# Optimization experiments

Hardware: AMD Instinct MI355X
Metric: run time of the kernel (lower is better)

The kernel has to match this reference:

```python
import jax, jax.numpy as jnp
import numpy as np

B, S, D = 2, 2048, 2048
NH, NKV, HD = 16, 4, 128
REP = NH // NKV
EPS = 1e-6
ROPE_THETA = 1e6


def setup_inputs() -> dict:
    key = jax.random.key(0)
    ks = jax.random.split(key, 6)
    x = jax.random.normal(ks[0], (B, S, D), jnp.float32)
    # real rotary embeddings: [S, HD]
    inv_freq = 1.0 / (ROPE_THETA ** (np.arange(0, HD, 2, dtype=np.float64) / HD))
    freqs = np.outer(np.arange(S, dtype=np.float64), inv_freq)
    emb = np.concatenate([freqs, freqs], axis=-1)
    cos = jnp.asarray(np.cos(emb), jnp.float32)
    sin = jnp.asarray(np.sin(emb), jnp.float32)
    scale = 1.0 / np.sqrt(D)
    Wq = jax.random.normal(ks[1], (D, NH * HD), jnp.float32) * scale   # [in, out]
    Wk = jax.random.normal(ks[2], (D, NKV * HD), jnp.float32) * scale
    Wv = jax.random.normal(ks[3], (D, NKV * HD), jnp.float32) * scale
    Wo = jax.random.normal(ks[4], (NH * HD, D), jnp.float32) * (1.0 / np.sqrt(NH * HD))
    q_norm_w = jnp.ones((HD,), jnp.float32)
    k_norm_w = jnp.ones((HD,), jnp.float32)
    return dict(x=x, cos=cos, sin=sin, Wq=Wq, Wk=Wk, Wv=Wv, Wo=Wo,
                q_norm_w=q_norm_w, k_norm_w=k_norm_w)


def _rms_norm(h, w):
    var = jnp.mean(h * h, axis=-1, keepdims=True)
    return w * (h * jax.lax.rsqrt(var + EPS))


def _rotate_half(h):
    h1, h2 = jnp.split(h, 2, axis=-1)
    return jnp.concatenate([-h2, h1], axis=-1)


def reference(x, cos, sin, Wq, Wk, Wv, Wo, q_norm_w, k_norm_w):
    b, s, _ = x.shape
    q = (x @ Wq).reshape(b, s, NH, HD)
    k = (x @ Wk).reshape(b, s, NKV, HD)
    v = (x @ Wv).reshape(b, s, NKV, HD)
    # per-head QK RMSNorm
    q = _rms_norm(q, q_norm_w)
    k = _rms_norm(k, k_norm_w)
    # RoPE: cos/sin [S,HD] -> broadcast over batch and heads
    c = cos[None, :, None, :]
    s_ = sin[None, :, None, :]
    q = q * c + _rotate_half(q) * s_
    k = k * c + _rotate_half(k) * s_
    # GQA: group q heads per kv head instead of materializing repeat_kv
    qg = q.reshape(b, s, NKV, REP, HD)
    scores = jnp.einsum('bqgrd,bkgd->bgrqk', qg, k) / np.sqrt(HD)
    causal = jnp.tril(jnp.ones((s, s), bool))  # [q,k]
    scores = jnp.where(causal, scores, -jnp.inf)
    probs = jax.nn.softmax(scores.astype(jnp.float32), axis=-1).astype(q.dtype)
    out = jnp.einsum('bgrqk,bkgd->bqgrd', probs, v).reshape(b, s, NH * HD)
    return out @ Wo
```

## Files before the change

kernel.cpp:

```cpp
#include <hip/hip_runtime.h>
#include <hip/hip_bf16.h>
#include <math.h>

#define B_ 2
#define S_ 2048
#define D_ 2048
#define NH_ 16
#define NKV_ 4
#define HD_ 128
#define EPS_ 1e-6f
#define SCALE_ 0.08838834764831845f
#define LOG2E_ 1.4426950408889634f
#define KOFF_ 2048
#define VOFF_ 2560
#define MINIT_ -1e30f

typedef float f32x4 __attribute__((ext_vector_type(4)));
typedef short bf16x8 __attribute__((ext_vector_type(8)));
typedef short short4v __attribute__((ext_vector_type(4)));
typedef float float4v __attribute__((ext_vector_type(4)));
typedef unsigned uint2v __attribute__((ext_vector_type(2)));
typedef unsigned uint4v __attribute__((ext_vector_type(4)));

static __device__ __forceinline__ short f2bf(float f) {
    union { float f; unsigned u; } x{f};
    unsigned r = (x.u + 0x7fff + ((x.u >> 16) & 1)) >> 16;
    return (short)r;
}
static __device__ __forceinline__ float bf2f(short s) {
    union { unsigned u; float f; } x; x.u = ((unsigned)(unsigned short)s) << 16; return x.f;
}
static __device__ __forceinline__ unsigned pack_bf2(float a, float b) {
    return __builtin_amdgcn_perm(__builtin_bit_cast(unsigned, b),
                                 __builtin_bit_cast(unsigned, a), 0x07060302u);
}

#define AS1(p) ((const __attribute__((address_space(1))) void*)(p))
#define AS3(p) ((__attribute__((address_space(3))) void*)(p))
static __device__ __forceinline__ void async16(const void* g, void* l) {
    __builtin_amdgcn_global_load_lds(AS1(g), AS3(l), 16, 0, 0);
}
#define SB_() __builtin_amdgcn_sched_barrier(0)

__global__ __launch_bounds__(256) void cast_kernel(const float* __restrict__ in,
                                                   short* __restrict__ out) {
    size_t i = ((size_t)blockIdx.x * 256 + threadIdx.x) * 4;
    float4v v = *(const float4v*)(in + i);
    short4v o; o.x = f2bf(v.x); o.y = f2bf(v.y); o.z = f2bf(v.z); o.w = f2bf(v.w);
    *(short4v*)(out + i) = o;
}

__global__ __launch_bounds__(256) void transpose_all_kernel(const float* __restrict__ Wq,
                                                            const float* __restrict__ Wk,
                                                            const float* __restrict__ Wv,
                                                            const float* __restrict__ Wo,
                                                            short* __restrict__ Wt,
                                                            short* __restrict__ Wot) {
    __shared__ float tile[64][65];
    const int bx = blockIdx.x, by = blockIdx.y;
    const float* src; short* dst; int N, nb;
    if (bx < 32)      { src = Wq; dst = Wt;                         N = 2048; nb = bx; }
    else if (bx < 40) { src = Wk; dst = Wt + (size_t)KOFF_ * 2048;  N = 512;  nb = bx - 32; }
    else if (bx < 48) { src = Wv; dst = Wt + (size_t)VOFF_ * 2048;  N = 512;  nb = bx - 40; }
    else              { src = Wo; dst = Wot;                        N = 2048; nb = bx - 48; }
    const int n0 = nb * 64, k0 = by * 64;
    const int tid = threadIdx.x;
    for (int r = 0; r < 16; ++r) {
        int k = r * 4 + (tid >> 6);
        int n = tid & 63;
        tile[k][n] = src[(size_t)(k0 + k) * N + n0 + n];
    }
    __syncthreads();
    for (int r = 0; r < 4; ++r) {
        int n  = r * 16 + (tid >> 4);
        int kk = (tid & 15) * 4;
        short4v o4;
        o4.x = f2bf(tile[kk + 0][n]); o4.y = f2bf(tile[kk + 1][n]);
        o4.z = f2bf(tile[kk + 2][n]); o4.w = f2bf(tile[kk + 3][n]);
        *(short4v*)&dst[(size_t)(n0 + n) * 2048 + k0 + kk] = o4;
    }
}

__global__ __launch_bounds__(512, 2) void gemm_oproj_kernel(const short* __restrict__ A,
                                                            const short* __restrict__ Bt,
                                                            float* __restrict__ C) {
    __shared__ __align__(16) short smem[49152];
    short* A0 = smem;
    short* A1 = smem + 8192;
    short* B0 = smem + 16384;
    short* B1 = smem + 32768;

    const int tid  = threadIdx.x;
    const int orig = blockIdx.y * 8 + blockIdx.x;
    const int swz  = (orig & 7) * 32 + (orig >> 3);
    const int bn = swz & 7, bm = swz >> 3;
    const int wave = tid >> 6, lane = tid & 63;
    const int quad = lane >> 4, l16 = lane & 15;
    const int wr = wave >> 2, wc = wave & 3;

    const short* Ag = A  + (size_t)(bm * 128) * 2048;
    const short* Bg = Bt + (size_t)(bn * 256) * 2048;

    f32x4 acc[4][4];
#pragma unroll
    for (int i = 0; i < 4; ++i)
#pragma unroll
        for (int j = 0; j < 4; ++j) acc[i][j] = (f32x4){0.f, 0.f, 0.f, 0.f};

    bf16x8 a[4][2], b0[2][2], b1[2][2];

    auto stage_half = [&](const short* gpanel, int t, int h, short* lslot) {
#pragma unroll
        for (int u = 0; u < 2; ++u) {
            int ci = u * 512 + tid;
            int r  = ci >> 3;
            int cb = ((ci & 7) * 16) ^ ((r & 7) << 4);
            async16(gpanel + (size_t)(h * 128 + r) * 2048 + t * 64 + (cb >> 1),
                    lslot + h * 8192 + ci * 8);
        }
    };

#define OLDA_(lbuf) \
    _Pragma("unroll") for (int mt = 0; mt < 4; ++mt) \
    _Pragma("unroll") for (int ks = 0; ks < 2; ++ks) { \
        int row_ = wr * 64 + mt * 16 + l16; \
        int cb_  = (ks * 64 + quad * 16) ^ ((row_ & 7) << 4); \
        a[mt][ks] = *(const bf16x8*)&(lbuf)[row_ * 64 + (cb_ >> 1)]; \
    }
#define OLDB_(lbuf, qn, breg) \
    _Pragma("unroll") for (int ntl = 0; ntl < 2; ++ntl) \
    _Pragma("unroll") for (int ks = 0; ks < 2; ++ks) { \
        int row_ = wc * 64 + (qn) * 32 + ntl * 16 + l16; \
        int cb_  = (ks * 64 + quad * 16) ^ ((row_ & 7) << 4); \
        breg[ntl][ks] = *(const bf16x8*)&(lbuf)[row_ * 64 + (cb_ >> 1)]; \
    }
#define OBAR_() __builtin_amdgcn_s_barrier()
#define OMFMA_(qn, breg) do { \
    __builtin_amdgcn_s_setprio(1); \
    _Pragma("unroll") for (int mt = 0; mt < 4; ++mt) \
    _Pragma("unroll") for (int ntl = 0; ntl < 2; ++ntl) \
    _Pragma("unroll") for (int ks = 0; ks < 2; ++ks) \
        acc[mt][(qn) * 2 + ntl] = __builtin_amdgcn_mfma_f32_16x16x32_bf16( \
            a[mt][ks], breg[ntl][ks], acc[mt][(qn) * 2 + ntl], 0, 0, 0); \
    __builtin_amdgcn_s_setprio(0); __builtin_amdgcn_s_barrier(); } while (0)

    stage_half(Bg, 0, 0, B0); stage_half(Bg, 0, 1, B0);
    stage_half(Ag, 0, 0, A0);
    asm volatile("s_waitcnt vmcnt(0)" ::: "memory");
    __builtin_amdgcn_s_barrier();

#pragma unroll 1
    for (int i = 0; i < 16; ++i) {
        const int tE = 2 * i, tO = 2 * i + 1;
        const bool more = (i < 15);

        stage_half(Ag, tO, 0, A1);
        stage_half(Bg, tO, 0, B1); stage_half(Bg, tO, 1, B1);
        OLDA_(A0); OLDB_(B0, 0, b0);
        OBAR_();
        OMFMA_(0, b0);

        if (more) {
            stage_half(Ag, tE + 2, 0, A0);
            asm volatile("s_waitcnt vmcnt(2)" ::: "memory");
        } else {
            asm volatile("s_waitcnt vmcnt(0)" ::: "memory");
        }
        OLDB_(B0, 1, b1);
        OBAR_();
        OMFMA_(1, b1);

        if (more) { stage_half(Bg, tE + 2, 0, B0); stage_half(Bg, tE + 2, 1, B0); }
        OLDA_(A1); OLDB_(B1, 0, b0);
        OBAR_();
        OMFMA_(0, b0);

        if (more) { asm volatile("s_waitcnt vmcnt(0)" ::: "memory"); }
        OLDB_(B1, 1, b1);
        OBAR_();
        OMFMA_(1, b1);
    }

#pragma unroll
    for (int mt = 0; mt < 4; ++mt)
#pragma unroll
        for (int nt = 0; nt < 4; ++nt)
#pragma unroll
            for (int j = 0; j < 4; ++j) {
                int row = bm * 128 + wr * 64 + mt * 16 + quad * 4 + j;
                int col = bn * 256 + wc * 64 + nt * 16 + l16;
                C[(size_t)row * 2048 + col] = acc[mt][nt][j];
            }
#undef OLDA_
#undef OLDB_
#undef OBAR_
#undef OMFMA_
}

#define QKV_ITERS 16

__global__ __launch_bounds__(512, 2) void qkv_fused_kernel(const short* __restrict__ xb,
                                                           const short* __restrict__ Wt,
                                                           const float* __restrict__ cosb,
                                                           const float* __restrict__ sinb,
                                                           const float* __restrict__ qw,
                                                           const float* __restrict__ kw,
                                                           short* __restrict__ q_rope,
                                                           short* __restrict__ k_rope,
                                                           short* __restrict__ vtr) {
    __shared__ __align__(16) short smem[65536];

    short* A0 = smem;
    short* A1 = smem + 8192;
    short* B0 = smem + 16384;
    short* B1 = smem + 40960;

    const int tid  = threadIdx.x;
    const int orig = blockIdx.y * 8 + blockIdx.x;
    const int swz  = (orig & 7) * 32 + (orig >> 3);
    const int bn = swz >> 5, bm = swz & 31;
    const int wave = tid >> 6, lane = tid & 63;
    const int quad = lane >> 4, l16 = lane & 15;
    const int wr = wave >> 2, wc = wave & 3;

    const short* Ag = xb + (size_t)(bm * 128) * 2048;
    const short* Bg = Wt + (size_t)(bn * 384) * 2048;

    f32x4 acc[4][6];
#pragma unroll
    for (int i = 0; i < 4; ++i)
#pragma unroll
        for (int j = 0; j < 6; ++j) acc[i][j] = (f32x4){0.f, 0.f, 0.f, 0.f};

    bf16x8 a[4][2], b0[3][2], b1[3][2];

    auto stage_half = [&](const short* gpanel, int t, int h, short* lslot) {
#pragma unroll
        for (int u = 0; u < 2; ++u) {
            int ci = u * 512 + tid;
            int r  = ci >> 3;
            int cb = ((ci & 7) * 16) ^ ((r & 7) << 4);
            async16(gpanel + (size_t)(h * 128 + r) * 2048 + t * 64 + (cb >> 1),
                    lslot + h * 8192 + ci * 8);
        }
    };

#define LDA_(lbuf) \
    _Pragma("unroll") for (int mt = 0; mt < 4; ++mt) \
    _Pragma("unroll") for (int ks = 0; ks < 2; ++ks) { \
        int row_ = wr * 64 + mt * 16 + l16; \
        int cb_  = (ks * 64 + quad * 16) ^ ((row_ & 7) << 4); \
        a[mt][ks] = *(const bf16x8*)&(lbuf)[row_ * 64 + (cb_ >> 1)]; \
    }
#define LDB_(lbuf, qn, breg) \
    _Pragma("unroll") for (int ntl = 0; ntl < 3; ++ntl) \
    _Pragma("unroll") for (int ks = 0; ks < 2; ++ks) { \
        int row_ = wc * 96 + (qn) * 48 + ntl * 16 + l16; \
        int cb_  = (ks * 64 + quad * 16) ^ ((row_ & 7) << 4); \
        breg[ntl][ks] = *(const bf16x8*)&(lbuf)[row_ * 64 + (cb_ >> 1)]; \
    }
#define PH_BAR() do { __builtin_amdgcn_sched_barrier(0); __builtin_amdgcn_s_barrier(); } while (0)
#define PH_MFMA24(qn, breg) do { \
        __builtin_amdgcn_s_setprio(1); \
        _Pragma("unroll") for (int mt = 0; mt < 4; ++mt) \
        _Pragma("unroll") for (int ntl = 0; ntl < 3; ++ntl) \
        _Pragma("unroll") for (int ks = 0; ks < 2; ++ks) \
            acc[mt][(qn) * 3 + ntl] = __builtin_amdgcn_mfma_f32_16x16x32_bf16( \
                a[mt][ks], breg[ntl][ks], acc[mt][(qn) * 3 + ntl], 0, 0, 0); \
        __builtin_amdgcn_s_setprio(0); \
        __builtin_amdgcn_sched_barrier(0); __builtin_amdgcn_s_barrier(); } while (0)

    stage_half(Bg, 0, 0, B0); stage_half(Bg, 0, 1, B0); stage_half(Bg, 0, 2, B0);
    stage_half(Ag, 0, 0, A0);
    stage_half(Ag, 1, 0, A1);
    asm volatile("s_waitcnt vmcnt(2)" ::: "memory");
    __builtin_amdgcn_s_barrier();

#pragma unroll 1
    for (int i = 0; i < QKV_ITERS; ++i) {
        const int tE = 2 * i, tO = 2 * i + 1;
        const bool more = (i < QKV_ITERS - 1);

        LDA_(A0); LDB_(B0, 0, b0);
        stage_half(Bg, tO, 0, B1); stage_half(Bg, tO, 1, B1); stage_half(Bg, tO, 2, B1);
        PH_BAR();
        PH_MFMA24(0, b0);

        LDB_(B0, 1, b1);
        if (more) {
            stage_half(Ag, tE + 2, 0, A0);
            asm volatile("s_waitcnt vmcnt(2)" ::: "memory");
        } else {
            asm volatile("s_waitcnt vmcnt(0)" ::: "memory");
        }
        PH_BAR();
        PH_MFMA24(1, b1);

        LDA_(A1); LDB_(B1, 0, b0);
        if (more) { stage_half(Bg, tE + 2, 0, B0); stage_half(Bg, tE + 2, 1, B0); stage_half(Bg, tE + 2, 2, B0); }
        PH_BAR();
        PH_MFMA24(0, b0);

        LDB_(B1, 1, b1);
        if (more) {
            stage_half(Ag, tO + 2, 0, A1);
            asm volatile("s_waitcnt vmcnt(2)" ::: "memory");
        }
        PH_BAR();
        PH_MFMA24(1, b1);
    }

#pragma unroll
    for (int mt = 0; mt < 4; ++mt) {
        int tok0 = bm * 128 + wr * 64 + mt * 16 + quad * 4;
        int bb = tok0 >> 11, s0 = tok0 & (S_ - 1);
#pragma unroll
        for (int nt = 0; nt < 6; ++nt) {
            int colh = wc * 96 + nt * 16;
            int gh = bn * 3 + (colh >> 7);
            if (gh >= 20) {
                int g = gh - 20;
                int d = (colh & 127) + l16;
                short4v o4;
                o4.x = f2bf(acc[mt][nt][0]); o4.y = f2bf(acc[mt][nt][1]);
                o4.z = f2bf(acc[mt][nt][2]); o4.w = f2bf(acc[mt][nt][3]);
                *(short4v*)&vtr[((size_t)(bb * NKV_ + g) * HD_ + d) * S_ + s0] = o4;
            }
        }
    }
    if (bn * 3 >= 20) return;

    short* ct = smem;
    float* ps = (float*)(smem + 49152);
    {
#pragma unroll
        for (int nt = 0; nt < 6; ++nt) {
            float s[4][4];
#pragma unroll
            for (int mt = 0; mt < 4; ++mt)
#pragma unroll
                for (int j = 0; j < 4; ++j)
                    s[mt][j] = acc[mt][nt][j] * acc[mt][nt][j];
#pragma unroll
            for (int off = 1; off < 16; off <<= 1)
#pragma unroll
                for (int mt = 0; mt < 4; ++mt)
#pragma unroll
                    for (int j = 0; j < 4; ++j)
                        s[mt][j] += __shfl_xor(s[mt][j], off);
            if (l16 == 0) {
#pragma unroll
                for (int mt = 0; mt < 4; ++mt)
#pragma unroll
                    for (int j = 0; j < 4; ++j)
                        ps[(wc * 6 + nt) * 128 + wr * 64 + mt * 16 + quad * 4 + j] = s[mt][j];
            }
        }
    }
#pragma unroll
    for (int mt = 0; mt < 4; ++mt)
#pragma unroll
        for (int nt = 0; nt < 6; ++nt)
#pragma unroll
            for (int j = 0; j < 4; ++j)
                ct[(wr * 64 + mt * 16 + quad * 4 + j) * 384 + wc * 96 + nt * 16 + l16]
                    = f2bf(acc[mt][nt][j]);
    __syncthreads();

#pragma unroll 1
    for (int it = 0; it < 12; ++it) {
        int f = it * 512 + tid;
        int seg = f & 15;
        int rh  = f >> 4;
        int row = rh & 127, head = rh >> 7;
        int gh = bn * 3 + head;
        if (gh >= 20) continue;
        const bool isQ = gh < 16;
        const float osc = isQ ? (SCALE_ * LOG2E_) : 1.0f;
        const float* w = isQ ? qw : kw;
        float ss = 0.f;
#pragma unroll
        for (int c = 0; c < 8; ++c) ss += ps[(head * 8 + c) * 128 + row];
        float rstd = rsqrtf(ss * (1.0f / HD_) + EPS_);
        int tok = bm * 128 + row;
        int bb = tok >> 11, s = tok & (S_ - 1);
        int c0 = seg * 8, p0 = (seg ^ 8) * 8;
        bf16x8 ta = *(const bf16x8*)&ct[row * 384 + head * 128 + c0];
        bf16x8 tb = *(const bf16x8*)&ct[row * 384 + head * 128 + p0];
        float sgn = (seg < 8) ? -1.0f : 1.0f;
        float4v cs0 = *(const float4v*)&cosb[(size_t)s * HD_ + c0];
        float4v cs1 = *(const float4v*)&cosb[(size_t)s * HD_ + c0 + 4];
        float4v sn0 = *(const float4v*)&sinb[(size_t)s * HD_ + c0];
        float4v sn1 = *(const float4v*)&sinb[(size_t)s * HD_ + c0 + 4];
        float ov[8];
#pragma unroll
        for (int i = 0; i < 8; ++i) {
            float n1 = bf2f(ta[i]) * rstd * w[c0 + i];
            float n2 = bf2f(tb[i]) * rstd * w[p0 + i];
            float cs = (i < 4) ? cs0[i & 3] : cs1[i & 3];
            float sn = (i < 4) ? sn0[i & 3] : sn1[i & 3];
            ov[i] = (n1 * cs + sgn * n2 * sn) * osc;
        }
        uint4v wv;
#pragma unroll
        for (int i2 = 0; i2 < 4; ++i2)
            wv[i2] = ((unsigned)(unsigned short)f2bf(ov[2 * i2])) |
                     ((unsigned)(unsigned short)f2bf(ov[2 * i2 + 1]) << 16);
        short* dst = isQ
            ? q_rope + ((size_t)(bb * S_ + s) * NH_ + gh) * HD_ + c0
            : k_rope + ((size_t)(bb * NKV_ + (gh - 16)) * S_ + s) * HD_ + c0;
        *(uint4v*)dst = wv;
    }
#undef LDA_
#undef LDB_
#undef PH_BAR
#undef PH_MFMA24
}

__global__ __launch_bounds__(512, 1) void attn_kernel(const short* __restrict__ qr,
                                                      const short* __restrict__ kg,
                                                      const short* __restrict__ vt,
                                                      short* __restrict__ aout) {
    __shared__ __align__(16) short Ks[2][2][8192];
    __shared__ __align__(16) short Vs[2][2][8192];

    const int lin = blockIdx.x;
    const int b  = lin & 1;
    const int g  = (lin >> 1) & 3;
    const int hq = (lin >> 3) & 3;
    const int pr = lin >> 5;
    const int h  = g * 4 + hq;

    const int wave = threadIdx.x >> 6, lane = threadIdx.x & 63;
    const int quad = lane >> 4, l16 = lane & 15;
    const int half = wave >> 2;
    const int ww   = wave & 3;

    const short* kbase = kg + (size_t)(b * NKV_ + g) * S_ * HD_;
    const short* vbase = vt + (size_t)(b * NKV_ + g) * HD_ * S_;

    auto stage = [&](int kt, short* Kd, short* Vd) {
        const short* kt_base = kbase + (size_t)kt * 64 * HD_;
        const short* vt_base = vbase + kt * 64;
#pragma unroll
        for (int t = 0; t < 2; ++t) {
            int ci  = (wave * 2 + t) * 64 + lane;
            int key = ci >> 4;
            int c   = (ci & 15) ^ ((key ^ (key >> 2)) & 15);
            async16(kt_base + key * HD_ + c * 8, Kd + ci * 8);
        }
#pragma unroll
        for (int t = 0; t < 2; ++t) {
            int ci = (wave * 2 + t) * 64 + lane;
            int d  = ci >> 3;
            int c  = (ci & 7) ^ (d & 7);
            async16(vt_base + (size_t)d * S_ + c * 8, Vd + ci * 8);
        }
    };

#pragma unroll 1
    for (int ph = 0; ph < 2; ++ph) {
        const int qt    = ph ? (15 - pr) : pr;
        const int nhalf = qt + 1;
        const int qrow0 = qt * 128 + ww * 16 + l16;
        const int qrow1 = qrow0 + 64;

        bf16x8 qf[2][4];
#pragma unroll
        for (int qs = 0; qs < 2; ++qs) {
            const short* qp = qr + ((size_t)(b * S_ + (qs ? qrow1 : qrow0)) * NH_ + h) * HD_;
#pragma unroll
            for (int ks = 0; ks < 4; ++ks)
                qf[qs][ks] = *(const bf16x8*)(qp + ks * 32 + quad * 8);
        }

        f32x4 o[2][8];
#pragma unroll
        for (int qs = 0; qs < 2; ++qs)
#pragma unroll
            for (int i = 0; i < 8; ++i) o[qs][i] = (f32x4){0.f, 0.f, 0.f, 0.f};
        float m_i[2] = {MINIT_, MINIT_};
        float l_i[2] = {0.f, 0.f};

        stage(0, Ks[0][0], Vs[0][0]);
        stage(1, Ks[1][0], Vs[1][0]);
        int buf = 0;
#pragma unroll 1
        for (int i = 0; i < nhalf; ++i) {
            __syncthreads();
            if (i + 1 < nhalf) {
                stage(2 * i + 2, Ks[0][buf ^ 1], Vs[0][buf ^ 1]);
                stage(2 * i + 3, Ks[1][buf ^ 1], Vs[1][buf ^ 1]);
            }
            const short* Kb = Ks[half][buf];
            const short* Vb = Vs[half][buf];
            const int ktm = 2 * i + half;

            f32x4 acc[2][4];
#pragma unroll
            for (int qs = 0; qs < 2; ++qs)
#pragma unroll
                for (int t = 0; t < 4; ++t) acc[qs][t] = (f32x4){0.f, 0.f, 0.f, 0.f};
            __builtin_amdgcn_s_setprio(1);
#pragma unroll
            for (int t = 0; t < 4; ++t) {
                int lk = ((t >> 1) << 5) + ((l16 >> 2) << 3) + ((t & 1) << 2) + (l16 & 3);
                const short* kp = &Kb[lk * 128];
                int pm = (lk ^ (lk >> 2)) & 15;
#pragma unroll
                for (int ks = 0; ks < 4; ++ks) {
                    bf16x8 kf = *(const bf16x8*)(kp + (((ks * 4 + quad) ^ pm) * 8));
                    acc[0][t] = __builtin_amdgcn_mfma_f32_16x16x32_bf16(kf, qf[0][ks], acc[0][t], 0, 0, 0);
                    acc[1][t] = __builtin_amdgcn_mfma_f32_16x16x32_bf16(kf, qf[1][ks], acc[1][t], 0, 0, 0);
                }
            }
            __builtin_amdgcn_s_setprio(0);
            const int key_base = ktm * 64;
#pragma unroll
            for (int qs = 0; qs < 2; ++qs) {
                int qmin = qt * 128 + qs * 64 + ww * 16;
                int qrow = qs ? qrow1 : qrow0;
                if (key_base + 63 > qmin) {
#pragma unroll
                    for (int t = 0; t < 4; ++t)
#pragma unroll
                        for (int j = 0; j < 4; ++j) {
                            int kl = key_base + ((t >> 1) << 5) + (quad << 3) + ((t & 1) << 2) + j;
                            if (kl > qrow) acc[qs][t][j] = -INFINITY;
                        }
                }
            }
            unsigned pk[2][2][4];
#pragma unroll
            for (int qs = 0; qs < 2; ++qs) {
                float mx = m_i[qs];
#pragma unroll
                for (int t = 0; t < 4; ++t)
#pragma unroll
                    for (int j = 0; j < 4; ++j) mx = fmaxf(mx, acc[qs][t][j]);
                mx = fmaxf(mx, __shfl_xor(mx, 16));
                mx = fmaxf(mx, __shfl_xor(mx, 32));
                float al = __builtin_amdgcn_exp2f(m_i[qs] - mx);
                m_i[qs] = mx;
                float rs = 0.f;
                float p[4][4];
#pragma unroll
                for (int t = 0; t < 4; ++t)
#pragma unroll
                    for (int j = 0; j < 4; ++j) {
                        float e = __builtin_amdgcn_exp2f(acc[qs][t][j] - mx);
                        p[t][j] = e;
                        rs += e;
                    }
                rs += __shfl_xor(rs, 16);
                rs += __shfl_xor(rs, 32);
                l_i[qs] = al * l_i[qs] + rs;
#pragma unroll
                for (int d8 = 0; d8 < 8; ++d8)
#pragma unroll
                    for (int j = 0; j < 4; ++j) o[qs][d8][j] *= al;
#pragma unroll
                for (int grp = 0; grp < 2; ++grp) {
                    pk[qs][grp][0] = pack_bf2(p[2 * grp][0],     p[2 * grp][1]);
                    pk[qs][grp][1] = pack_bf2(p[2 * grp][2],     p[2 * grp][3]);
                    pk[qs][grp][2] = pack_bf2(p[2 * grp + 1][0], p[2 * grp + 1][1]);
                    pk[qs][grp][3] = pack_bf2(p[2 * grp + 1][2], p[2 * grp + 1][3]);
                }
            }
            __builtin_amdgcn_s_setprio(1);
#pragma unroll
            for (int grp = 0; grp < 2; ++grp) {
                union { unsigned u[4]; bf16x8 v; } pb0, pb1;
#pragma unroll
                for (int i2 = 0; i2 < 4; ++i2) { pb0.u[i2] = pk[0][grp][i2]; pb1.u[i2] = pk[1][grp][i2]; }
#pragma unroll
                for (int d8 = 0; d8 < 8; ++d8) {
                    int d = d8 * 16 + l16;
                    bf16x8 vf = *(const bf16x8*)&Vb[d * 64 + (((grp * 4 + quad) ^ (d & 7)) * 8)];
                    o[0][d8] = __builtin_amdgcn_mfma_f32_16x16x32_bf16(vf, pb0.v, o[0][d8], 0, 0, 0);
                    o[1][d8] = __builtin_amdgcn_mfma_f32_16x16x32_bf16(vf, pb1.v, o[1][d8], 0, 0, 0);
                }
            }
            __builtin_amdgcn_s_setprio(0);
            buf ^= 1;
        }

        __syncthreads();
        float* exch = (float*)(ww < 2 ? &Ks[0][0][0] : &Vs[0][0][0]);
        float* slot = exch + ((size_t)((ww & 1) * 64 + lane) * 68);
        if (half == 1) {
#pragma unroll
            for (int qs = 0; qs < 2; ++qs) {
#pragma unroll
                for (int d8 = 0; d8 < 8; ++d8)
#pragma unroll
                    for (int j = 0; j < 4; ++j)
                        slot[qs * 32 + d8 * 4 + j] = o[qs][d8][j];
                slot[64 + qs] = m_i[qs];
                slot[66 + qs] = l_i[qs];
            }
        }
        __syncthreads();
        if (half == 0) {
#pragma unroll
            for (int qs = 0; qs < 2; ++qs) {
                float mB = slot[64 + qs], lB = slot[66 + qs];
                float m  = fmaxf(m_i[qs], mB);
                float wA = __builtin_amdgcn_exp2f(m_i[qs] - m);
                float wB = __builtin_amdgcn_exp2f(mB - m);
                float il = 1.0f / (l_i[qs] * wA + lB * wB);
                int qrow = qs ? qrow1 : qrow0;
                short* op = aout + ((size_t)(b * S_ + qrow) * NH_ + h) * HD_ + quad * 4;
#pragma unroll
                for (int d8 = 0; d8 < 8; ++d8) {
                    float v0 = (o[qs][d8][0] * wA + slot[qs * 32 + d8 * 4 + 0] * wB) * il;
                    float v1 = (o[qs][d8][1] * wA + slot[qs * 32 + d8 * 4 + 1] * wB) * il;
                    float v2 = (o[qs][d8][2] * wA + slot[qs * 32 + d8 * 4 + 2] * wB) * il;
                    float v3 = (o[qs][d8][3] * wA + slot[qs * 32 + d8 * 4 + 3] * wB) * il;
                    uint2v wv;
                    wv.x = ((unsigned)(unsigned short)f2bf(v0)) |
                           ((unsigned)(unsigned short)f2bf(v1) << 16);
                    wv.y = ((unsigned)(unsigned short)f2bf(v2)) |
                           ((unsigned)(unsigned short)f2bf(v3) << 16);
                    *(uint2v*)(op + d8 * 16) = wv;
                }
            }
        }
        __syncthreads();
    }
}

extern "C" void kernel_launch(void* const* d_in, const int* in_sizes, int n_in,
                              void* d_out, int out_size, void* d_ws, size_t ws_size,
                              hipStream_t stream) {
    (void)in_sizes; (void)n_in; (void)out_size; (void)ws_size;
    const float* x    = (const float*)d_in[0];
    const float* cosb = (const float*)d_in[1];
    const float* sinb = (const float*)d_in[2];
    const float* Wq   = (const float*)d_in[3];
    const float* Wk   = (const float*)d_in[4];
    const float* Wv   = (const float*)d_in[5];
    const float* Wo   = (const float*)d_in[6];
    const float* qw   = (const float*)d_in[7];
    const float* kw   = (const float*)d_in[8];
    float* out = (float*)d_out;

    char* ws = (char*)d_ws;
    short* xb     = (short*)ws;  ws += (size_t)4096 * 2048 * 2;
    short* Wt     = (short*)ws;  ws += (size_t)3072 * 2048 * 2;
    short* Wot    = (short*)ws;  ws += (size_t)2048 * 2048 * 2;
    short* q_rope = (short*)ws;  ws += (size_t)4096 * 2048 * 2;
    short* k_rope = (short*)ws;  ws += (size_t)4096 * 512 * 2;
    short* vt     = (short*)ws;  ws += (size_t)4096 * 512 * 2;
    short* a_out  = (short*)ws;  ws += (size_t)4096 * 2048 * 2;

    const int M = B_ * S_;

    cast_kernel<<<M * 2048 / 1024, 256, 0, stream>>>(x, xb);
    transpose_all_kernel<<<dim3(80, 32), 256, 0, stream>>>(Wq, Wk, Wv, Wo, Wt, Wot);

    qkv_fused_kernel<<<dim3(8, 32), 512, 0, stream>>>(
        xb, Wt, cosb, sinb, qw, kw, q_rope, k_rope, vt);

    attn_kernel<<<256, 512, 0, stream>>>(q_rope, k_rope, vt, a_out);

    gemm_oproj_kernel<<<dim3(8, 32), 512, 0, stream>>>(a_out, Wot, out);
}
```

Baseline: 279.1 us.

## Merge cast and transpose kernels, remap QKV tiles per XCD, defer softmax rescale

The activation cast and weight transpose kernels are combined into one launch, with extra blocks doing the cast, which saves a kernel launch and lets the two run concurrently. The QKV GEMM block index mapping is changed so that each XCD gets a contiguous group of row tiles across all column tiles, aiming for better L2 reuse of activations. In attention, the online softmax skips updating the running max and rescaling the output accumulator when the new block max stays within a threshold of the old one. That skip relies on exp2 headroom in fp32 and bf16 P values up to 2^8, and adds a wave-wide vote per block.

```diff
diff --git a/kernel.cpp b/kernel.cpp
--- a/kernel.cpp
+++ b/kernel.cpp
@@ -42,29 +42,31 @@
 }
 #define SB_() __builtin_amdgcn_sched_barrier(0)
 
-__global__ __launch_bounds__(256) void cast_kernel(const float* __restrict__ in,
-                                                   short* __restrict__ out) {
-    size_t i = ((size_t)blockIdx.x * 256 + threadIdx.x) * 4;
-    float4v v = *(const float4v*)(in + i);
-    short4v o; o.x = f2bf(v.x); o.y = f2bf(v.y); o.z = f2bf(v.z); o.w = f2bf(v.w);
-    *(short4v*)(out + i) = o;
-}
-
-__global__ __launch_bounds__(256) void transpose_all_kernel(const float* __restrict__ Wq,
-                                                            const float* __restrict__ Wk,
-                                                            const float* __restrict__ Wv,
-                                                            const float* __restrict__ Wo,
-                                                            short* __restrict__ Wt,
-                                                            short* __restrict__ Wot) {
+__global__ __launch_bounds__(256) void prep_kernel(const float* __restrict__ x,
+                                                   short* __restrict__ xb,
+                                                   const float* __restrict__ Wq,
+                                                   const float* __restrict__ Wk,
+                                                   const float* __restrict__ Wv,
+                                                   const float* __restrict__ Wo,
+                                                   short* __restrict__ Wt,
+                                                   short* __restrict__ Wot) {
     __shared__ float tile[64][65];
     const int bx = blockIdx.x, by = blockIdx.y;
+    const int tid = threadIdx.x;
+    if (bx >= 80) {
+        int cb = (bx - 80) * 32 + by;
+        size_t i = ((size_t)cb * 256 + tid) * 4;
+        float4v v = *(const float4v*)(x + i);
+        short4v o; o.x = f2bf(v.x); o.y = f2bf(v.y); o.z = f2bf(v.z); o.w = f2bf(v.w);
+        *(short4v*)(xb + i) = o;
+        return;
+    }
     const float* src; short* dst; int N, nb;
     if (bx < 32)      { src = Wq; dst = Wt;                         N = 2048; nb = bx; }
     else if (bx < 40) { src = Wk; dst = Wt + (size_t)KOFF_ * 2048;  N = 512;  nb = bx - 32; }
     else if (bx < 48) { src = Wv; dst = Wt + (size_t)VOFF_ * 2048;  N = 512;  nb = bx - 40; }
     else              { src = Wo; dst = Wot;                        N = 2048; nb = bx - 48; }
     const int n0 = nb * 64, k0 = by * 64;
-    const int tid = threadIdx.x;
     for (int r = 0; r < 16; ++r) {
         int k = r * 4 + (tid >> 6);
         int n = tid & 63;
@@ -217,8 +219,10 @@
 
     const int tid  = threadIdx.x;
     const int orig = blockIdx.y * 8 + blockIdx.x;
-    const int swz  = (orig & 7) * 32 + (orig >> 3);
-    const int bn = swz >> 5, bm = swz & 31;
+    const int xcd  = orig & 7;
+    const int idx  = orig >> 3;
+    const int bm   = xcd * 4 + (idx & 3);
+    const int bn   = idx >> 2;
     const int wave = tid >> 6, lane = tid & 63;
     const int quad = lane >> 4, l16 = lane & 15;
     const int wr = wave >> 2, wc = wave & 3;
@@ -533,15 +537,21 @@
             unsigned pk[2][2][4];
 #pragma unroll
             for (int qs = 0; qs < 2; ++qs) {
-                float mx = m_i[qs];
+                float pm = -INFINITY;
 #pragma unroll
                 for (int t = 0; t < 4; ++t)
 #pragma unroll
-                    for (int j = 0; j < 4; ++j) mx = fmaxf(mx, acc[qs][t][j]);
-                mx = fmaxf(mx, __shfl_xor(mx, 16));
-                mx = fmaxf(mx, __shfl_xor(mx, 32));
-                float al = __builtin_amdgcn_exp2f(m_i[qs] - mx);
-                m_i[qs] = mx;
+                    for (int j = 0; j < 4; ++j) pm = fmaxf(pm, acc[qs][t][j]);
+                pm = fmaxf(pm, __shfl_xor(pm, 16));
+                pm = fmaxf(pm, __shfl_xor(pm, 32));
+                bool defer = __all(pm <= m_i[qs] + 8.0f);
+                float mx, al;
+                if (defer) { mx = m_i[qs]; al = 1.0f; }
+                else {
+                    mx = fmaxf(pm, m_i[qs]);
+                    al = __builtin_amdgcn_exp2f(m_i[qs] - mx);
+                    m_i[qs] = mx;
+                }
                 float rs = 0.f;
                 float p[4][4];
 #pragma unroll
@@ -555,10 +565,12 @@
                 rs += __shfl_xor(rs, 16);
                 rs += __shfl_xor(rs, 32);
                 l_i[qs] = al * l_i[qs] + rs;
-#pragma unroll
-                for (int d8 = 0; d8 < 8; ++d8)
-#pragma unroll
-                    for (int j = 0; j < 4; ++j) o[qs][d8][j] *= al;
+                if (!defer) {
+#pragma unroll
+                    for (int d8 = 0; d8 < 8; ++d8)
+#pragma unroll
+                        for (int j = 0; j < 4; ++j) o[qs][d8][j] *= al;
+                }
 #pragma unroll
                 for (int grp = 0; grp < 2; ++grp) {
                     pk[qs][grp][0] = pack_bf2(p[2 * grp][0],     p[2 * grp][1]);
@@ -654,10 +666,7 @@
     short* vt     = (short*)ws;  ws += (size_t)4096 * 512 * 2;
     short* a_out  = (short*)ws;  ws += (size_t)4096 * 2048 * 2;
 
-    const int M = B_ * S_;
-
-    cast_kernel<<<M * 2048 / 1024, 256, 0, stream>>>(x, xb);
-    transpose_all_kernel<<<dim3(80, 32), 256, 0, stream>>>(Wq, Wk, Wv, Wo, Wt, Wot);
+    prep_kernel<<<dim3(336, 32), 256, 0, stream>>>(x, xb, Wq, Wk, Wv, Wo, Wt, Wot);
 
     qkv_fused_kernel<<<dim3(8, 32), 512, 0, stream>>>(
         xb, Wt, cosb, sinb, qw, kw, q_rope, k_rope, vt);
```

Result: no change. 283.4 us (+1.5%).
